# Performance work log

Hardware: AMD Instinct MI355X
Metric: run time of the kernel (lower is better)

## Reference

```python
import jax, jax.numpy as jnp
import numpy as np

N, E, F_IN, HID, HEADS, OUT, NGRAPH = 50000, 800000, 128, 64, 4, 64, 512
NEG_SLOPE = 0.2


def setup_inputs() -> dict:
    key = jax.random.key(0)
    ks = jax.random.split(key, 16)
    d1 = HID * HEADS  # 256
    inp = {
        "x": jax.random.normal(ks[0], (N, F_IN), jnp.float32),
        "edge_index": jax.random.randint(ks[1], (2, E), 0, N, jnp.int64),
        "batch": jnp.sort(jax.random.randint(ks[2], (N,), 0, NGRAPH, jnp.int64)),
        # layer 1 params (GATConv(F_IN -> HID, heads=HEADS, concat=True))
        "W1": jax.random.normal(ks[3], (F_IN, d1), jnp.float32) * 0.05,
        "att_src1": jax.random.normal(ks[4], (HEADS, HID), jnp.float32) * 0.05,
        "att_dst1": jax.random.normal(ks[5], (HEADS, HID), jnp.float32) * 0.05,
        "b1": jnp.zeros((d1,), jnp.float32),
        # layer 2 params (GATConv(d1 -> HID, heads=HEADS, concat=True))
        "W2": jax.random.normal(ks[6], (d1, d1), jnp.float32) * 0.05,
        "att_src2": jax.random.normal(ks[7], (HEADS, HID), jnp.float32) * 0.05,
        "att_dst2": jax.random.normal(ks[8], (HEADS, HID), jnp.float32) * 0.05,
        "b2": jnp.zeros((d1,), jnp.float32),
        # final linear
        "fc_w": jax.random.normal(ks[9], (d1, OUT), jnp.float32) * 0.05,
        "fc_b": jnp.zeros((OUT,), jnp.float32),
    }
    return inp


def _gat_layer(x, src, dst, W, att_src, att_dst, bias):
    # linear transform, split into heads: [N, H, C]
    h = (x @ W).reshape(N, HEADS, HID)
    # per-node attention logits (a^T h), per head: [N, H]
    a_s = jnp.einsum("nhc,hc->nh", h, att_src)
    a_d = jnp.einsum("nhc,hc->nh", h, att_dst)
    # per-edge logits with leaky relu: [E', H]
    e = a_s[src] + a_d[dst]
    e = jnp.where(e > 0, e, NEG_SLOPE * e)
    # segment softmax over edges grouped by destination node
    m = jax.ops.segment_max(e, dst, num_segments=N)
    ex = jnp.exp(e - m[dst])
    s = jax.ops.segment_sum(ex, dst, num_segments=N)
    alpha = ex / s[dst]  # every node has a self-loop -> s > 0
    # weighted message aggregation: scatter-add of alpha * h_src
    out = jax.ops.segment_sum(h[src] * alpha[:, :, None], dst, num_segments=N)
    return out.reshape(N, HEADS * HID) + bias


def reference(x, edge_index, batch, W1, att_src1, att_dst1, b1,
              W2, att_src2, att_dst2, b2, fc_w, fc_b):
    # PyG GATConv default add_self_loops=True
    loop = jnp.arange(N, dtype=edge_index.dtype)
    src = jnp.concatenate([edge_index[0], loop])
    dst = jnp.concatenate([edge_index[1], loop])

    h = _gat_layer(x, src, dst, W1, att_src1, att_dst1, b1)
    h = jax.nn.elu(h)  # dropout is identity in eval mode
    h = _gat_layer(h, src, dst, W2, att_src2, att_dst2, b2)
    h = jax.nn.elu(h)

    # global mean pool over graphs
    sums = jax.ops.segment_sum(h, batch, num_segments=NGRAPH)
    cnts = jax.ops.segment_sum(jnp.ones((N,), h.dtype), batch, num_segments=NGRAPH)
    pooled = sums / jnp.maximum(cnts, 1.0)[:, None]

    return pooled @ fc_w + fc_b
```

## Files before the change

### kernel.cpp

```cpp
#include <hip/hip_runtime.h>
#include <cstddef>
#include <cstdint>

#define NN 50000
#define EE 800000
#define FIN 128
#define D1 256
#define HID 64
#define HEADS 4
#define NG 512
#define FOUT 64
#define NEG_SLOPE 0.2f
#define CAP 96


typedef _Float16 f16x8 __attribute__((ext_vector_type(8)));
typedef _Float16 f16x4 __attribute__((ext_vector_type(4)));
typedef float f32x4 __attribute__((ext_vector_type(4)));

__device__ __forceinline__ float leaky(float x) { return x > 0.f ? x : NEG_SLOPE * x; }

__global__ void k_scatter_direct(const int* __restrict__ ei, int* __restrict__ cnt,
                                 unsigned short* __restrict__ slot) {
    int i = (blockIdx.x * 256 + threadIdx.x) * 2;
    if (i < EE) {
        const int2 s2 = *(const int2*)(ei + i);
        const int2 d2 = *(const int2*)(ei + EE + i);
        int p0 = atomicAdd(&cnt[d2.x], 1);
        if (p0 < CAP)
            __builtin_nontemporal_store((unsigned short)s2.x,
                                        &slot[(size_t)d2.x * CAP + p0]);
        int p1 = atomicAdd(&cnt[d2.y], 1);
        if (p1 < CAP)
            __builtin_nontemporal_store((unsigned short)s2.y,
                                        &slot[(size_t)d2.y * CAP + p1]);
    }
}

__global__ void k_cvt_w(const float* __restrict__ W1, const float* __restrict__ W2,
                        _Float16* __restrict__ w1t, _Float16* __restrict__ w2t) {
    int idx = blockIdx.x * 256 + threadIdx.x;
    if (idx < 256 * FIN) {
        int n = idx / FIN, k = idx - n * FIN;
        w1t[idx] = (_Float16)W1[(size_t)k * 256 + n];
    } else if (idx < 256 * FIN + 256 * D1) {
        int j = idx - 256 * FIN;
        int n = j >> 8, k = j & 255;
        w2t[j] = (_Float16)W2[(size_t)k * 256 + n];
    }
}

#define BM 128
#define BN 128
#define BK 64
#define LDK (BK + 4)

template <int K, typename AT>
__global__ __launch_bounds__(256) void k_gemm(const AT* __restrict__ A,
                                              const _Float16* __restrict__ Bt,
                                              _Float16* __restrict__ C,
                                              const float* __restrict__ att_s,
                                              const float* __restrict__ att_d,
                                              float* __restrict__ a_s,
                                              float* __restrict__ a_d) {
    __shared__ _Float16 As[BM][LDK];
    __shared__ _Float16 Bs[BN][LDK];
    const int tid = threadIdx.x;
    const int lane = tid & 63;
    const int wave = tid >> 6;
    const int wm = wave & 1, wn = wave >> 1;
    const int m0 = blockIdx.x * BM;
    const int n0 = blockIdx.y * BN;
    const int row_m = lane & 15, quad = lane >> 4;

    f32x4 acc[4][4];
#pragma unroll
    for (int mi = 0; mi < 4; ++mi)
#pragma unroll
        for (int ni = 0; ni < 4; ++ni)
#pragma unroll
            for (int r = 0; r < 4; ++r) acc[mi][ni][r] = 0.f;

    const int c8 = (tid & 7) * 8;
    const int rr = tid >> 3;

    for (int k0 = 0; k0 < K; k0 += BK) {
#pragma unroll
        for (int p = 0; p < 4; ++p) {
            int r = p * 32 + rr;
            int gr = m0 + r; gr = gr < NN ? gr : NN - 1;
            f16x8 o;
            if constexpr (sizeof(AT) == 4) {
                const float4 v0 = *(const float4*)((const float*)A + (size_t)gr * K + k0 + c8);
                const float4 v1 = *(const float4*)((const float*)A + (size_t)gr * K + k0 + c8 + 4);
                o[0] = (_Float16)v0.x; o[1] = (_Float16)v0.y;
                o[2] = (_Float16)v0.z; o[3] = (_Float16)v0.w;
                o[4] = (_Float16)v1.x; o[5] = (_Float16)v1.y;
                o[6] = (_Float16)v1.z; o[7] = (_Float16)v1.w;
            } else {
                o = *(const f16x8*)((const _Float16*)A + (size_t)gr * K + k0 + c8);
            }
            *(f16x8*)(&As[r][c8]) = o;
        }
#pragma unroll
        for (int p = 0; p < 4; ++p) {
            int r = p * 32 + rr;
            f16x8 v = *(const f16x8*)(Bt + (size_t)(n0 + r) * K + k0 + c8);
            *(f16x8*)(&Bs[r][c8]) = v;
        }
        __syncthreads();
#pragma unroll
        for (int kc = 0; kc < BK; kc += 32) {
            f16x8 af[4], bf[4];
#pragma unroll
            for (int mi = 0; mi < 4; ++mi)
                af[mi] = *(const f16x8*)(&As[wm * 64 + mi * 16 + row_m][kc + quad * 8]);
#pragma unroll
            for (int ni = 0; ni < 4; ++ni)
                bf[ni] = *(const f16x8*)(&Bs[wn * 64 + ni * 16 + row_m][kc + quad * 8]);
#pragma unroll
            for (int mi = 0; mi < 4; ++mi)
#pragma unroll
                for (int ni = 0; ni < 4; ++ni)
                    acc[mi][ni] = __builtin_amdgcn_mfma_f32_16x16x32_f16(
                        bf[ni], af[mi], acc[mi][ni], 0, 0, 0);
        }
        __syncthreads();
    }
#pragma unroll
    for (int mi = 0; mi < 4; ++mi) {
        int m = m0 + wm * 64 + mi * 16 + row_m;
        if (m < NN) {
#pragma unroll
            for (int ni = 0; ni < 4; ++ni) {
                f16x4 o;
                o[0] = (_Float16)acc[mi][ni][0];
                o[1] = (_Float16)acc[mi][ni][1];
                o[2] = (_Float16)acc[mi][ni][2];
                o[3] = (_Float16)acc[mi][ni][3];
                *(f16x4*)(C + (size_t)m * D1 + n0 + wn * 64 + ni * 16 + quad * 4) = o;
            }
        }
    }
    const int head = blockIdx.y * 2 + wn;
    const float* attsv = att_s + head * HID;
    const float* attdv = att_d + head * HID;
    float avs[4][4], avd[4][4];
#pragma unroll
    for (int ni = 0; ni < 4; ++ni)
#pragma unroll
        for (int r = 0; r < 4; ++r) {
            avs[ni][r] = attsv[ni * 16 + quad * 4 + r];
            avd[ni][r] = attdv[ni * 16 + quad * 4 + r];
        }
#pragma unroll
    for (int mi = 0; mi < 4; ++mi) {
        float ps = 0.f, pd = 0.f;
#pragma unroll
        for (int ni = 0; ni < 4; ++ni)
#pragma unroll
            for (int r = 0; r < 4; ++r) {
                ps += acc[mi][ni][r] * avs[ni][r];
                pd += acc[mi][ni][r] * avd[ni][r];
            }
        ps += __shfl_xor(ps, 16); ps += __shfl_xor(ps, 32);
        pd += __shfl_xor(pd, 16); pd += __shfl_xor(pd, 32);
        int m = m0 + wm * 64 + mi * 16 + row_m;
        if (quad == 0 && m < NN) {
            a_s[m * 4 + head] = ps;
            a_d[m * 4 + head] = pd;
        }
    }
}

__global__ __launch_bounds__(64) void k_aggregate(
    const _Float16* __restrict__ h, const float* __restrict__ a_s,
    const float* __restrict__ a_d, const int* __restrict__ cnt,
    const unsigned short* __restrict__ slot, const float* __restrict__ bias,
    _Float16* __restrict__ out, int apply_elu) {
    const int n = blockIdx.x;
    const int tid = threadIdx.x;
    const int myhead = tid >> 4;
    const int c4 = tid * 4;
    const int start = n * CAP;
    const int deg = cnt[n];
    const int end = start + (deg < CAP ? deg : CAP);

    __shared__ float s_w[64][4];

    const float4 ad = *(const float4*)(a_d + (size_t)n * 4);

    const float4 asn = *(const float4*)(a_s + (size_t)n * 4);
    float w0 = __expf(leaky(asn.x + ad.x));
    float w1 = __expf(leaky(asn.y + ad.y));
    float w2 = __expf(leaky(asn.z + ad.z));
    float w3 = __expf(leaky(asn.w + ad.w));
    const float wself = (myhead == 0) ? w0 : (myhead == 1) ? w1 : (myhead == 2) ? w2 : w3;
    const f16x4 hn = *(const f16x4*)(h + ((size_t)n << 8) + c4);
    float l = wself;
    float4 acc = make_float4(wself * (float)hn[0], wself * (float)hn[1],
                             wself * (float)hn[2], wself * (float)hn[3]);

    for (int base = start; base < end; base += 64) {
        const int len = min(64, end - base);
        if (tid < len) {
            const int s = (int)slot[base + tid];
            const float4 as = *(const float4*)(a_s + (size_t)s * 4);
            s_w[tid][0] = __expf(leaky(as.x + ad.x));
            s_w[tid][1] = __expf(leaky(as.y + ad.y));
            s_w[tid][2] = __expf(leaky(as.z + ad.z));
            s_w[tid][3] = __expf(leaky(as.w + ad.w));
        }
        __syncthreads();
#pragma unroll 4
        for (int jj = 0; jj < len; ++jj) {
            const int s = (int)slot[base + jj];
            const float w = s_w[jj][myhead];
            const f16x4 hv = *(const f16x4*)(h + ((size_t)s << 8) + c4);
            l += w;
            acc.x += w * (float)hv[0];
            acc.y += w * (float)hv[1];
            acc.z += w * (float)hv[2];
            acc.w += w * (float)hv[3];
        }
        __syncthreads();
    }
    const float inv = 1.f / l;
    const float4 bb = *(const float4*)(bias + c4);
    float vx = acc.x * inv + bb.x;
    float vy = acc.y * inv + bb.y;
    float vz = acc.z * inv + bb.z;
    float vw = acc.w * inv + bb.w;
    if (apply_elu) {
        vx = vx > 0.f ? vx : expm1f(vx);
        vy = vy > 0.f ? vy : expm1f(vy);
        vz = vz > 0.f ? vz : expm1f(vz);
        vw = vw > 0.f ? vw : expm1f(vw);
    }
    f16x4 o;
    o[0] = (_Float16)vx; o[1] = (_Float16)vy; o[2] = (_Float16)vz; o[3] = (_Float16)vw;
    *(f16x4*)(out + (size_t)n * D1 + c4) = o;
}

__global__ __launch_bounds__(256) void k_pool_fc(const _Float16* __restrict__ h,
                                                 const int* __restrict__ batch,
                                                 const float* __restrict__ fc_w,
                                                 const float* __restrict__ fc_b,
                                                 float* __restrict__ out) {
    __shared__ float srow[4][D1];
    __shared__ float row[D1];
    const int g = blockIdx.x, tid = threadIdx.x;
    const int w = tid >> 6, lane = tid & 63;
    const int c4 = lane * 4;

    int lo = 0, hi = NN;
    while (lo < hi) { int mid = (lo + hi) >> 1; if (batch[mid] < g) lo = mid + 1; else hi = mid; }
    int start = lo;
    hi = NN;
    while (lo < hi) { int mid = (lo + hi) >> 1; if (batch[mid] < g + 1) lo = mid + 1; else hi = mid; }
    int end = lo;

    float a0 = 0.f, a1 = 0.f, a2 = 0.f, a3 = 0.f;
    for (int n = start + w; n < end; n += 4) {
        const f16x4 v = *(const f16x4*)(h + (size_t)n * D1 + c4);
        a0 += (float)v[0]; a1 += (float)v[1];
        a2 += (float)v[2]; a3 += (float)v[3];
    }
    srow[w][c4 + 0] = a0; srow[w][c4 + 1] = a1;
    srow[w][c4 + 2] = a2; srow[w][c4 + 3] = a3;
    __syncthreads();
    const float inv = 1.f / fmaxf((float)(end - start), 1.f);
    row[tid] = (srow[0][tid] + srow[1][tid] + srow[2][tid] + srow[3][tid]) * inv;
    __syncthreads();
    if (tid < FOUT) {
        float o = 0.f;
#pragma unroll 4
        for (int k = 0; k < D1; ++k) o += row[k] * fc_w[k * FOUT + tid];
        out[(size_t)g * FOUT + tid] = o + fc_b[tid];
    }
}

extern "C" void kernel_launch(void* const* d_in, const int* in_sizes, int n_in,
                              void* d_out, int out_size, void* d_ws, size_t ws_size,
                              hipStream_t stream) {
    const float* x        = (const float*)d_in[0];
    const int*   ei       = (const int*)d_in[1];
    const int*   batch    = (const int*)d_in[2];
    const float* W1       = (const float*)d_in[3];
    const float* att_src1 = (const float*)d_in[4];
    const float* att_dst1 = (const float*)d_in[5];
    const float* b1       = (const float*)d_in[6];
    const float* W2       = (const float*)d_in[7];
    const float* att_src2 = (const float*)d_in[8];
    const float* att_dst2 = (const float*)d_in[9];
    const float* b2       = (const float*)d_in[10];
    const float* fc_w     = (const float*)d_in[11];
    const float* fc_b     = (const float*)d_in[12];
    float* out = (float*)d_out;

    _Float16* h_pre  = (_Float16*)d_ws;
    _Float16* h_act  = h_pre + (size_t)NN * D1;
    _Float16* w1t    = h_act + (size_t)NN * D1;
    _Float16* w2t    = w1t + 256 * FIN;
    float* a_s       = (float*)(w2t + 256 * D1);
    float* a_d       = a_s + (size_t)NN * 4;
    int*   cnt       = (int*)(a_d + (size_t)NN * 4);
    unsigned short* slot16 = (unsigned short*)(cnt + NN);

    hipMemsetAsync(cnt, 0, NN * sizeof(int), stream);
    k_scatter_direct<<<(EE / 2 + 255) / 256, 256, 0, stream>>>(ei, cnt, slot16);

    k_cvt_w<<<(256 * (FIN + D1) + 255) / 256, 256, 0, stream>>>(W1, W2, w1t, w2t);

    dim3 ggrid((NN + BM - 1) / BM, D1 / BN);

    k_gemm<FIN, float><<<ggrid, 256, 0, stream>>>(x, w1t, h_pre,
                                                  att_src1, att_dst1, a_s, a_d);
    k_aggregate<<<NN, 64, 0, stream>>>(h_pre, a_s, a_d, cnt, slot16, b1, h_act, 1);

    k_gemm<D1, _Float16><<<ggrid, 256, 0, stream>>>(h_act, w2t, h_pre,
                                                    att_src2, att_dst2, a_s, a_d);
    k_aggregate<<<NN, 64, 0, stream>>>(h_pre, a_s, a_d, cnt, slot16, b2, h_act, 1);

    k_pool_fc<<<NG, 256, 0, stream>>>(h_act, batch, fc_w, fc_b, out);
}
```

Baseline: 349.4 us.

## Fold count memset into weight-convert kernel, widen scatter, use fast exp ELU

Replaces the hipMemsetAsync of the per-node counters with a zeroing step inside the weight-conversion kernel, so one launch goes away. The edge scatter now loads four edges per thread with int4 loads instead of two. ELU uses __expf(x)-1 instead of expm1f, and the pooling loop gets an unroll pragma. The fast exp loses some precision near zero, and the per-thread chain of atomics in the scatter gets longer.

Result: no change. 345.1 us (-1.2%).

```diff
diff --git a/kernel.cpp b/kernel.cpp
--- a/kernel.cpp
+++ b/kernel.cpp
@@ -20,26 +20,11 @@
 
 __device__ __forceinline__ float leaky(float x) { return x > 0.f ? x : NEG_SLOPE * x; }
 
-__global__ void k_scatter_direct(const int* __restrict__ ei, int* __restrict__ cnt,
-                                 unsigned short* __restrict__ slot) {
-    int i = (blockIdx.x * 256 + threadIdx.x) * 2;
-    if (i < EE) {
-        const int2 s2 = *(const int2*)(ei + i);
-        const int2 d2 = *(const int2*)(ei + EE + i);
-        int p0 = atomicAdd(&cnt[d2.x], 1);
-        if (p0 < CAP)
-            __builtin_nontemporal_store((unsigned short)s2.x,
-                                        &slot[(size_t)d2.x * CAP + p0]);
-        int p1 = atomicAdd(&cnt[d2.y], 1);
-        if (p1 < CAP)
-            __builtin_nontemporal_store((unsigned short)s2.y,
-                                        &slot[(size_t)d2.y * CAP + p1]);
-    }
-}
-
-__global__ void k_cvt_w(const float* __restrict__ W1, const float* __restrict__ W2,
-                        _Float16* __restrict__ w1t, _Float16* __restrict__ w2t) {
+__global__ void k_prep(const float* __restrict__ W1, const float* __restrict__ W2,
+                       _Float16* __restrict__ w1t, _Float16* __restrict__ w2t,
+                       int* __restrict__ cnt) {
     int idx = blockIdx.x * 256 + threadIdx.x;
+    if (idx < NN) cnt[idx] = 0;
     if (idx < 256 * FIN) {
         int n = idx / FIN, k = idx - n * FIN;
         w1t[idx] = (_Float16)W1[(size_t)k * 256 + n];
@@ -47,6 +32,28 @@
         int j = idx - 256 * FIN;
         int n = j >> 8, k = j & 255;
         w2t[j] = (_Float16)W2[(size_t)k * 256 + n];
+    }
+}
+
+__global__ void k_scatter_direct(const int* __restrict__ ei, int* __restrict__ cnt,
+                                 unsigned short* __restrict__ slot) {
+    int i = (blockIdx.x * 256 + threadIdx.x) * 4;
+    if (i < EE) {
+        const int4 s4 = *(const int4*)(ei + i);
+        const int4 d4 = *(const int4*)(ei + EE + i);
+        int p;
+        p = atomicAdd(&cnt[d4.x], 1);
+        if (p < CAP) __builtin_nontemporal_store((unsigned short)s4.x,
+                                                 &slot[(size_t)d4.x * CAP + p]);
+        p = atomicAdd(&cnt[d4.y], 1);
+        if (p < CAP) __builtin_nontemporal_store((unsigned short)s4.y,
+                                                 &slot[(size_t)d4.y * CAP + p]);
+        p = atomicAdd(&cnt[d4.z], 1);
+        if (p < CAP) __builtin_nontemporal_store((unsigned short)s4.z,
+                                                 &slot[(size_t)d4.z * CAP + p]);
+        p = atomicAdd(&cnt[d4.w], 1);
+        if (p < CAP) __builtin_nontemporal_store((unsigned short)s4.w,
+                                                 &slot[(size_t)d4.w * CAP + p]);
     }
 }
 
@@ -232,10 +239,10 @@
     float vz = acc.z * inv + bb.z;
     float vw = acc.w * inv + bb.w;
     if (apply_elu) {
-        vx = vx > 0.f ? vx : expm1f(vx);
-        vy = vy > 0.f ? vy : expm1f(vy);
-        vz = vz > 0.f ? vz : expm1f(vz);
-        vw = vw > 0.f ? vw : expm1f(vw);
+        vx = vx > 0.f ? vx : __expf(vx) - 1.f;
+        vy = vy > 0.f ? vy : __expf(vy) - 1.f;
+        vz = vz > 0.f ? vz : __expf(vz) - 1.f;
+        vw = vw > 0.f ? vw : __expf(vw) - 1.f;
     }
     f16x4 o;
     o[0] = (_Float16)vx; o[1] = (_Float16)vy; o[2] = (_Float16)vz; o[3] = (_Float16)vw;
@@ -261,6 +268,7 @@
     int end = lo;
 
     float a0 = 0.f, a1 = 0.f, a2 = 0.f, a3 = 0.f;
+#pragma unroll 4
     for (int n = start + w; n < end; n += 4) {
         const f16x4 v = *(const f16x4*)(h + (size_t)n * D1 + c4);
         a0 += (float)v[0]; a1 += (float)v[1];
@@ -307,10 +315,9 @@
     int*   cnt       = (int*)(a_d + (size_t)NN * 4);
     unsigned short* slot16 = (unsigned short*)(cnt + NN);
 
-    hipMemsetAsync(cnt, 0, NN * sizeof(int), stream);
-    k_scatter_direct<<<(EE / 2 + 255) / 256, 256, 0, stream>>>(ei, cnt, slot16);
-
-    k_cvt_w<<<(256 * (FIN + D1) + 255) / 256, 256, 0, stream>>>(W1, W2, w1t, w2t);
+    k_prep<<<(256 * (FIN + D1) + 255) / 256, 256, 0, stream>>>(W1, W2, w1t, w2t, cnt);
+
+    k_scatter_direct<<<(EE / 4 + 255) / 256, 256, 0, stream>>>(ei, cnt, slot16);
 
     dim3 ggrid((NN + BM - 1) / BM, D1 / BN);
 
```
